# Kernel tuning notes

Measured on AMD Instinct MI355X. Metric: run time of the kernel, lower is better.

## Reference

```python
import jax, jax.numpy as jnp
import numpy as np

DECAY = 0.999
EPS = 1e-5
COMMIT = 0.25
ORTHO_W = 10.0
NUM_ORTHO = 128


def setup_inputs() -> dict:
    key = jax.random.key(0)
    k1, k2 = jax.random.split(key)
    M, D = 2048, 512
    B, T = 32, 1024
    x = jax.random.normal(k1, (B, T, D), dtype=jnp.float32)
    init_bound = 1.0 / M
    emb = jax.random.uniform(k2, (M, D), minval=-init_bound, maxval=init_bound, dtype=jnp.float32)
    return {
        "x": x,
        "embedding": emb,
        "ema_count": jnp.zeros((M,), jnp.float32),
        "ema_weight": emb,  # torch init: ema_weight = embedding.clone()
    }


def reference(x, embedding, ema_count, ema_weight):
    M, D = embedding.shape
    x_sg = jax.lax.stop_gradient(x)
    x_flat = x_sg.reshape(-1, D)  # [N, D]

    distances = (jnp.sum(embedding * embedding, axis=1)[None, :]
                 + jnp.sum(x_flat * x_flat, axis=1, keepdims=True)
                 - 2.0 * (x_flat @ embedding.T))
    indices = jnp.argmin(distances.astype(jnp.float32), axis=-1)  # [N]

    quantized = embedding[indices].reshape(x.shape)

    # EMA updates (training=True). one_hot(indices).sum(0) == scatter-add counts;
    # encodings.T @ x_flat == scatter-add of x rows into code slots.
    counts = jnp.zeros((M,), x.dtype).at[indices].add(1.0)
    new_count = DECAY * ema_count + (1.0 - DECAY) * counts
    n = jnp.sum(new_count)
    new_count = (new_count + EPS) / (n + M * EPS) * n
    dw = jnp.zeros((M, D), x.dtype).at[indices].add(x_flat)
    new_weight = DECAY * ema_weight + (1.0 - DECAY) * dw
    new_embedding = new_weight / new_count[:, None]

    codebook_loss = jnp.mean((x_sg - quantized) ** 2)
    e_latent_loss = jnp.mean((x - jax.lax.stop_gradient(quantized)) ** 2)
    commitment_loss = COMMIT * e_latent_loss

    quant_st = x + jax.lax.stop_gradient(quantized - x)  # straight-through

    # ortho loss over used codes of the UPDATED codebook (torch: self.embedding post-EMA).
    # Deterministic jit-safe variant of unique+randperm: take the first NUM_ORTHO
    # used code ids (stable argsort puts used codes first), mask padding if fewer.
    used = counts > 0
    order = jnp.argsort(jnp.where(used, 0, 1).astype(jnp.int32))  # stable sort
    sel = order[:NUM_ORTHO]
    valid = used[sel].astype(x.dtype)  # [NUM_ORTHO]
    codebk = new_embedding[sel]
    norm = jnp.maximum(jnp.linalg.norm(codebk, axis=-1, keepdims=True), 1e-12)
    normed = (codebk / norm) * valid[:, None]
    cosine_sim = normed @ normed.T
    n_valid = jnp.sum(valid)
    ortho_loss = jnp.sum((cosine_sim - jnp.diag(valid)) ** 2) / (n_valid * n_valid) * ORTHO_W

    return (quant_st, commitment_loss, codebook_loss, ortho_loss, indices,
            new_embedding, new_count, new_weight)
```

## Files before the change

kernel.cpp:

```cpp
#include <hip/hip_runtime.h>
#include <math.h>

#define N_ROWS 32768
#define M_CODES 2048
#define D_DIM 512
#define MARGIN 1.2e-3f
#define CAND_CAP 32

#define OUT_QST       0
#define OUT_COMMIT    16777216
#define OUT_CODEBOOK  16777217
#define OUT_ORTHO     16777218
#define OUT_INDICES   16777219
#define OUT_NEWEMB    16809987
#define OUT_NEWCOUNT  17858563
#define OUT_NEWW      17860611

#define WS_COUNTS     0
#define WS_CURSOR     2048
#define WS_SSE        4096
#define WS_ORTHO      4097
#define WS_CANDCNT    4104
#define WS_ZERO_FLOATS 36872
#define WS_E2         36872
#define WS_X2         38920
#define WS_IDX        71688
#define WS_NCN        104456
#define WS_SEL        106504
#define WS_VALID      106632
#define WS_NVALID     106760
#define WS_NORMED     106768
#define WS_NORMEDT    172304
#define WS_OFFS       237840
#define WS_ORDER      239896
#define WS_CANDC      272664
#define WS_CANDD      1321240
#define WS_XH         2369816
#define WS_EH         10758424
#define WS_TOTAL_FLOATS 11282712

typedef __attribute__((ext_vector_type(8))) short short8v;
typedef __attribute__((ext_vector_type(4))) float f32x4;

__device__ __forceinline__ unsigned short f2bf(float f) {
    unsigned u = __float_as_uint(f);
    unsigned r = (u + 0x7fffu + ((u >> 16) & 1u)) >> 16;
    return (unsigned short)r;
}

#define GLOAD16(g, s) __builtin_amdgcn_global_load_lds( \
    (const __attribute__((address_space(1))) void*)(g), \
    (__attribute__((address_space(3))) void*)(s), 16, 0, 0)

__global__ __launch_bounds__(256) void prep_kernel(const float* __restrict__ emb,
                                                   const float* __restrict__ x,
                                                   float* __restrict__ e2,
                                                   float* __restrict__ x2,
                                                   unsigned short* __restrict__ xh,
                                                   unsigned short* __restrict__ eh) {
    int row  = blockIdx.x * 4 + (threadIdx.x >> 6);
    int lane = threadIdx.x & 63;
    bool is_e = row < M_CODES;
    const float* src = is_e ? (emb + (size_t)row * D_DIM)
                            : (x + (size_t)(row - M_CODES) * D_DIM);
    unsigned short* dh = is_e ? (eh + (size_t)row * D_DIM)
                              : (xh + (size_t)(row - M_CODES) * D_DIM);
    float4 a = *(const float4*)(src + lane * 4);
    float4 b = *(const float4*)(src + 256 + lane * 4);
    float s = a.x*a.x + a.y*a.y + a.z*a.z + a.w*a.w
            + b.x*b.x + b.y*b.y + b.z*b.z + b.w*b.w;
#pragma unroll
    for (int o = 32; o > 0; o >>= 1) s += __shfl_xor(s, o, 64);

    ushort4 h0, h1;
    h0.x = f2bf(a.x); h0.y = f2bf(a.y); h0.z = f2bf(a.z); h0.w = f2bf(a.w);
    h1.x = f2bf(b.x); h1.y = f2bf(b.y); h1.z = f2bf(b.z); h1.w = f2bf(b.w);
    *(ushort4*)(dh + lane * 4)       = h0;
    *(ushort4*)(dh + 256 + lane * 4) = h1;

    if (lane == 0) {
        if (is_e) e2[row] = s;
        else      x2[row - M_CODES] = s;
    }
}

__global__ __launch_bounds__(256) void sq_kernel(const float* __restrict__ emb,
                                                 const float* __restrict__ x,
                                                 float* __restrict__ e2,
                                                 float* __restrict__ x2) {
    int row  = blockIdx.x * 4 + (threadIdx.x >> 6);
    int lane = threadIdx.x & 63;
    const float* src = (row < M_CODES) ? (emb + (size_t)row * D_DIM)
                                       : (x + (size_t)(row - M_CODES) * D_DIM);
    float4 a = *(const float4*)(src + lane * 4);
    float4 b = *(const float4*)(src + 256 + lane * 4);
    float s = a.x*a.x + a.y*a.y + a.z*a.z + a.w*a.w
            + b.x*b.x + b.y*b.y + b.z*b.z + b.w*b.w;
#pragma unroll
    for (int o = 32; o > 0; o >>= 1) s += __shfl_xor(s, o, 64);
    if (lane == 0) {
        if (row < M_CODES) e2[row] = s;
        else               x2[row - M_CODES] = s;
    }
}

__global__ __launch_bounds__(256, 1) void approx5_kernel(const unsigned short* __restrict__ xh,
                                                         const unsigned short* __restrict__ eh,
                                                         const float* __restrict__ e2g,
                                                         int* __restrict__ candcnt,
                                                         int* __restrict__ candC,
                                                         float* __restrict__ candD) {
    __shared__ short Bh[2][32768];

    const int t  = threadIdx.x;
    const int w  = t >> 6;
    const int l  = t & 63;
    const int ml = l & 15;
    const int q  = l >> 4;

    const int row0 = blockIdx.x * 128;
    const int wrow = row0 + w * 32;

    short8v af[2][16];
#pragma unroll
    for (int mi = 0; mi < 2; ++mi) {
        const unsigned short* ar = xh + (size_t)(wrow + mi * 16 + ml) * D_DIM + q * 8;
#pragma unroll
        for (int kk = 0; kk < 16; ++kk)
            af[mi][kk] = *(const short8v*)(ar + kk * 32);
    }

#define STAGE_B(buf, ch) do {                                                   \
    const int cb_ = (ch) * 64;                                                  \
    _Pragma("unroll")                                                           \
    for (int j_ = 0; j_ < 16; ++j_) {                                           \
        int c_ = w * 16 + j_;                                                   \
        GLOAD16(eh + (size_t)(cb_ + c_) * D_DIM + ((l ^ (c_ & 7)) * 8),         \
                &Bh[(buf)][c_ * 512]);                                          \
    }                                                                           \
} while (0)

    float rmin[2][4];
#pragma unroll
    for (int mi = 0; mi < 2; ++mi)
#pragma unroll
        for (int r = 0; r < 4; ++r) rmin[mi][r] = 3.0e38f;

    STAGE_B(0, 0);
    __syncthreads();
    int cur = 0;

    for (int ch = 0; ch < 32; ++ch) {
        if (ch < 31) STAGE_B(cur ^ 1, ch + 1);

        const int code0 = ch * 64;
        const short* Bb = &Bh[cur][0];

        f32x4 acc[2][4];
#pragma unroll
        for (int mi = 0; mi < 2; ++mi)
#pragma unroll
            for (int ni = 0; ni < 4; ++ni) acc[mi][ni] = (f32x4)0.f;

#pragma unroll
        for (int kk = 0; kk < 16; ++kk) {
#pragma unroll
            for (int ni = 0; ni < 4; ++ni) {
                const int c = ni * 16 + ml;
                short8v b = *(const short8v*)(Bb + c * 512 + (((kk * 4 + q) ^ (c & 7)) << 3));
                acc[0][ni] = __builtin_amdgcn_mfma_f32_16x16x32_bf16(af[0][kk], b, acc[0][ni], 0, 0, 0);
                acc[1][ni] = __builtin_amdgcn_mfma_f32_16x16x32_bf16(af[1][kk], b, acc[1][ni], 0, 0, 0);
            }
        }

        float e2v[4];
#pragma unroll
        for (int ni = 0; ni < 4; ++ni) e2v[ni] = e2g[code0 + ni * 16 + ml];

#pragma unroll
        for (int mi = 0; mi < 2; ++mi)
#pragma unroll
            for (int r = 0; r < 4; ++r) {
                float v = fminf(fminf(e2v[0] - 2.0f * acc[mi][0][r],
                                      e2v[1] - 2.0f * acc[mi][1][r]),
                                fminf(e2v[2] - 2.0f * acc[mi][2][r],
                                      e2v[3] - 2.0f * acc[mi][3][r]));
#pragma unroll
                for (int o = 1; o < 16; o <<= 1) v = fminf(v, __shfl_xor(v, o, 64));
                rmin[mi][r] = fminf(rmin[mi][r], v);
                const float rm = rmin[mi][r] + MARGIN;
                const int row_g = wrow + mi * 16 + q * 4 + r;
#pragma unroll
                for (int ni = 0; ni < 4; ++ni) {
                    float dd = e2v[ni] - 2.0f * acc[mi][ni][r];
                    if (dd <= rm) {
                        int pos = atomicAdd(&candcnt[row_g], 1);
                        if (pos < CAND_CAP) {
                            candC[row_g * CAND_CAP + pos] = code0 + ni * 16 + ml;
                            candD[row_g * CAND_CAP + pos] = dd;
                        }
                    }
                }
            }

        __syncthreads();
        cur ^= 1;
    }
#undef STAGE_B
}

__global__ __launch_bounds__(256) void rerank_kernel(const float* __restrict__ x,
                                                     const float* __restrict__ emb,
                                                     const float* __restrict__ e2,
                                                     const float* __restrict__ x2,
                                                     const int* __restrict__ candcnt,
                                                     const int* __restrict__ candC,
                                                     const float* __restrict__ candD,
                                                     float* __restrict__ counts,
                                                     int* __restrict__ idx_out,
                                                     float* __restrict__ idxf_out) {
    const int w = threadIdx.x >> 6;
    const int lane = threadIdx.x & 63;
    const int row = blockIdx.x * 4 + w;

    int cnt = candcnt[row];
    int best_c;

    if (cnt > CAND_CAP) {
        const float x2r = x2[row];
        const float* xr = x + (size_t)row * D_DIM;
        float bd = 3.0e38f;
        int   bc = 0x7fffffff;
        for (int c = lane; c < M_CODES; c += 64) {
            const float* er = emb + (size_t)c * D_DIM;
            float dot = 0.f;
            for (int k = 0; k < D_DIM; ++k) dot = fmaf(xr[k], er[k], dot);
            float d = (x2r + e2[c]) - 2.0f * dot;
            if (d < bd || (d == bd && c < bc)) { bd = d; bc = c; }
        }
#pragma unroll
        for (int o = 32; o > 0; o >>= 1) {
            float od = __shfl_xor(bd, o, 64);
            int   oc = __shfl_xor(bc, o, 64);
            if (od < bd || (od == bd && oc < bc)) { bd = od; bc = oc; }
        }
        best_c = bc;
    } else {
        float d = 3.0e38f;
        int   c = 0x7fffffff;
        if (lane < cnt) {
            d = candD[row * CAND_CAP + lane];
            c = candC[row * CAND_CAP + lane];
        }
        float dmin = d;
#pragma unroll
        for (int o = 32; o > 0; o >>= 1) dmin = fminf(dmin, __shfl_xor(dmin, o, 64));

        bool surv = (lane < cnt) && (d <= dmin + MARGIN);
        unsigned long long mask = __ballot(surv);

        if (__popcll(mask) == 1) {
            int src = __ffsll((long long)mask) - 1;
            best_c = __shfl(c, src, 64);
        } else {
            const float x2r = x2[row];
            const float* xr = x + (size_t)row * D_DIM;
            float4 xa = *(const float4*)(xr + lane * 8);
            float4 xb = *(const float4*)(xr + lane * 8 + 4);
            float bd = 3.0e38f;
            int   bc = 0x7fffffff;
            unsigned long long m = mask;
            while (m) {
                int src = __ffsll((long long)m) - 1;
                m &= m - 1;
                int cs = __shfl(c, src, 64);
                const float* er = emb + (size_t)cs * D_DIM;
                float4 ea = *(const float4*)(er + lane * 8);
                float4 eb = *(const float4*)(er + lane * 8 + 4);
                float dot = xa.x*ea.x + xa.y*ea.y + xa.z*ea.z + xa.w*ea.w
                          + xb.x*eb.x + xb.y*eb.y + xb.z*eb.z + xb.w*eb.w;
#pragma unroll
                for (int o = 32; o > 0; o >>= 1) dot += __shfl_xor(dot, o, 64);
                float t1 = x2r + e2[cs];
                float dex = t1 - 2.0f * dot;
                if (dex < bd || (dex == bd && cs < bc)) { bd = dex; bc = cs; }
            }
            best_c = bc;
        }
    }
    if (lane == 0) {
        idx_out[row] = best_c;
        idxf_out[row] = (float)best_c;
        atomicAdd(&counts[best_c], 1.0f);
    }
}

__global__ __launch_bounds__(256) void argmin_kernel(const float* __restrict__ x,
                                                     const float* __restrict__ emb,
                                                     const float* __restrict__ e2,
                                                     const float* __restrict__ x2,
                                                     int* __restrict__ idx_out,
                                                     float* __restrict__ idxf_out) {
    __shared__ float As[64][36];
    __shared__ float Bs[32][68];
    __shared__ float e2s[64];
    __shared__ float redD[64][17];
    __shared__ int   redI[64][17];

    const int t  = threadIdx.x;
    const int tx = t & 15;
    const int ty = t >> 4;
    const int row0 = blockIdx.x * 64;

    float rmin[4];
    int   ridx[4];
#pragma unroll
    for (int r = 0; r < 4; ++r) { rmin[r] = 3.0e38f; ridx[r] = 0; }

    float x2r[4];
#pragma unroll
    for (int r = 0; r < 4; ++r) x2r[r] = x2[row0 + ty * 4 + r];

    const int lr = t >> 3;
    const int lc = t & 7;

    for (int m0 = 0; m0 < M_CODES; m0 += 64) {
        __syncthreads();
        if (t < 64) e2s[t] = e2[m0 + t];

        float acc[4][4];
#pragma unroll
        for (int r = 0; r < 4; ++r)
#pragma unroll
            for (int c = 0; c < 4; ++c) acc[r][c] = 0.f;

        for (int k0 = 0; k0 < D_DIM; k0 += 32) {
            __syncthreads();
#pragma unroll
            for (int p = 0; p < 2; ++p) {
                int r = p * 32 + lr;
                float4 v = *(const float4*)(x + (size_t)(row0 + r) * D_DIM + k0 + lc * 4);
                *(float4*)(&As[r][lc * 4]) = v;
            }
#pragma unroll
            for (int p = 0; p < 2; ++p) {
                int r = p * 32 + lr;
                float4 v = *(const float4*)(emb + (size_t)(m0 + r) * D_DIM + k0 + lc * 4);
                Bs[lc * 4 + 0][r] = v.x;
                Bs[lc * 4 + 1][r] = v.y;
                Bs[lc * 4 + 2][r] = v.z;
                Bs[lc * 4 + 3][r] = v.w;
            }
            __syncthreads();

#pragma unroll
            for (int kk = 0; kk < 32; kk += 4) {
                float av[4][4], bv[4][4];
#pragma unroll
                for (int r = 0; r < 4; ++r) {
                    float4 a4 = *(const float4*)(&As[ty * 4 + r][kk]);
                    av[r][0] = a4.x; av[r][1] = a4.y; av[r][2] = a4.z; av[r][3] = a4.w;
                }
#pragma unroll
                for (int j = 0; j < 4; ++j) {
                    float4 b4 = *(const float4*)(&Bs[kk + j][tx * 4]);
                    bv[j][0] = b4.x; bv[j][1] = b4.y; bv[j][2] = b4.z; bv[j][3] = b4.w;
                }
#pragma unroll
                for (int j = 0; j < 4; ++j)
#pragma unroll
                    for (int r = 0; r < 4; ++r)
#pragma unroll
                        for (int c = 0; c < 4; ++c)
                            acc[r][c] += av[r][j] * bv[j][c];
            }
        }

#pragma unroll
        for (int c = 0; c < 4; ++c) {
            int mm = tx * 4 + c;
            int m  = m0 + mm;
            float e2v = e2s[mm];
#pragma unroll
            for (int r = 0; r < 4; ++r) {
                float t1 = x2r[r] + e2v;
                float dd  = t1 - 2.0f * acc[r][c];
                if (dd < rmin[r]) { rmin[r] = dd; ridx[r] = m; }
            }
        }
    }

    __syncthreads();
#pragma unroll
    for (int r = 0; r < 4; ++r) {
        redD[ty * 4 + r][tx] = rmin[r];
        redI[ty * 4 + r][tx] = ridx[r];
    }
    __syncthreads();
    if (t < 64) {
        float best = redD[t][0];
        int   bi   = redI[t][0];
#pragma unroll
        for (int i = 1; i < 16; ++i) {
            float dd = redD[t][i];
            int   ii = redI[t][i];
            if (dd < best || (dd == best && ii < bi)) { best = dd; bi = ii; }
        }
        idx_out[row0 + t]  = bi;
        idxf_out[row0 + t] = (float)bi;
    }
}

__global__ __launch_bounds__(256) void hist_kernel(const int* __restrict__ idx,
                                                   float* __restrict__ counts) {
    int r = blockIdx.x * 256 + threadIdx.x;
    atomicAdd(&counts[idx[r]], 1.0f);
}

__global__ __launch_bounds__(256) void qst_sse_kernel(const float* __restrict__ x,
                                                      const float* __restrict__ emb,
                                                      const int* __restrict__ idx,
                                                      float* __restrict__ sse,
                                                      float* __restrict__ qst) {
    const int w    = threadIdx.x >> 6;
    const int lane = threadIdx.x & 63;
    const int rowbase = blockIdx.x * 16 + w * 4;
    float loss = 0.f;
    for (int i = 0; i < 4; ++i) {
        const int row = rowbase + i;
        const int m   = idx[row];
#pragma unroll
        for (int j = 0; j < 2; ++j) {
            const int off = j * 256 + lane * 4;
            float4 xv = *(const float4*)(x + (size_t)row * D_DIM + off);
            float4 qv = *(const float4*)(emb + (size_t)m * D_DIM + off);
            float4 qs;
            qs.x = xv.x + (qv.x - xv.x);
            qs.y = xv.y + (qv.y - xv.y);
            qs.z = xv.z + (qv.z - xv.z);
            qs.w = xv.w + (qv.w - xv.w);
            *(float4*)(qst + (size_t)row * D_DIM + off) = qs;
            float dx;
            dx = xv.x - qv.x; loss += dx * dx;
            dx = xv.y - qv.y; loss += dx * dx;
            dx = xv.z - qv.z; loss += dx * dx;
            dx = xv.w - qv.w; loss += dx * dx;
        }
    }
#pragma unroll
    for (int o = 32; o > 0; o >>= 1) loss += __shfl_xor(loss, o, 64);
    if (lane == 0) atomicAdd(sse, loss);
}

__global__ __launch_bounds__(256) void f1_kernel(const float* __restrict__ ema_count,
                                                 const float* __restrict__ counts,
                                                 float* __restrict__ out_newcount,
                                                 float* __restrict__ nc_ws) {
    __shared__ float red[256];
    int t = threadIdx.x;
    float raw[8];
    float part = 0.f;
#pragma unroll
    for (int i = 0; i < 8; ++i) {
        int m = t * 8 + i;
        raw[i] = 0.999f * ema_count[m] + 0.001f * counts[m];
        part += raw[i];
    }
    red[t] = part;
    __syncthreads();
    for (int s = 128; s > 0; s >>= 1) {
        if (t < s) red[t] += red[t + s];
        __syncthreads();
    }
    float n = red[0];
    float denom = n + (float)M_CODES * 1e-5f;
#pragma unroll
    for (int i = 0; i < 8; ++i) {
        int m = t * 8 + i;
        float v = (raw[i] + 1e-5f) / denom * n;
        out_newcount[m] = v;
        nc_ws[m] = v;
    }
}

__global__ __launch_bounds__(256) void scan_kernel(const float* __restrict__ counts,
                                                   int* __restrict__ offs) {
    __shared__ int pre[257];
    int t = threadIdx.x;
    int c[8];
    int s = 0;
#pragma unroll
    for (int i = 0; i < 8; ++i) { c[i] = (int)counts[t * 8 + i]; s += c[i]; }
    pre[t] = s;
    __syncthreads();
    if (t == 0) {
        int run = 0;
        for (int i = 0; i < 256; ++i) { int v = pre[i]; pre[i] = run; run += v; }
        pre[256] = run;
    }
    __syncthreads();
    int base = pre[t];
#pragma unroll
    for (int i = 0; i < 8; ++i) { offs[t * 8 + i] = base; base += c[i]; }
}

__global__ __launch_bounds__(256) void fill_kernel(const int* __restrict__ idx,
                                                   const int* __restrict__ offs,
                                                   int* __restrict__ cursor,
                                                   int* __restrict__ order) {
    int r = blockIdx.x * 256 + threadIdx.x;
    int m = idx[r];
    int pos = atomicAdd(&cursor[m], 1);
    order[offs[m] + pos] = r;
}

__global__ __launch_bounds__(256) void gather_nw_kernel(const float* __restrict__ x,
                                                        const float* __restrict__ ema_weight,
                                                        const float* __restrict__ ncn,
                                                        const float* __restrict__ counts,
                                                        const int* __restrict__ offs,
                                                        const int* __restrict__ order,
                                                        float* __restrict__ out_ne,
                                                        float* __restrict__ out_nw) {
    const int m = blockIdx.x;
    const int t = threadIdx.x;
    const int beg = offs[m];
    const int end = beg + (int)counts[m];
    float ax = 0.f, ay = 0.f;
    for (int j = beg; j < end; ++j) {
        int r = order[j];
        float2 v = *(const float2*)(x + (size_t)r * D_DIM + t * 2);
        ax += v.x; ay += v.y;
    }
    size_t i = (size_t)m * D_DIM + t * 2;
    float2 wv = *(const float2*)(ema_weight + i);
    float  c  = ncn[m];
    float2 nw, ne;
    nw.x = 0.999f * wv.x + 0.001f * ax; ne.x = nw.x / c;
    nw.y = 0.999f * wv.y + 0.001f * ay; ne.y = nw.y / c;
    *(float2*)(out_nw + i) = nw;
    *(float2*)(out_ne + i) = ne;
}

__global__ __launch_bounds__(256) void g1_kernel(const float* __restrict__ counts,
                                                 const float* __restrict__ new_emb,
                                                 int* __restrict__ sel,
                                                 float* __restrict__ valid,
                                                 float* __restrict__ n_valid,
                                                 float* __restrict__ normed,
                                                 float* __restrict__ normedT) {
    __shared__ int pre[257];
    int t = threadIdx.x;
    int u = 0;
#pragma unroll
    for (int i = 0; i < 8; ++i) u += (counts[t * 8 + i] > 0.f) ? 1 : 0;
    pre[t] = u;
    __syncthreads();
    if (t == 0) {
        int run = 0;
        for (int i = 0; i < 256; ++i) { int c = pre[i]; pre[i] = run; run += c; }
        pre[256] = run;
    }
    __syncthreads();
    int U = pre[256];
    int base = pre[t];
    int run = 0;
    for (int i = 0; i < 8; ++i) {
        int m = t * 8 + i;
        bool used = counts[m] > 0.f;
        int ur = base + run;
        if (used) {
            if (ur < 128) sel[ur] = m;
            run++;
        } else {
            int pos = U + (m - ur);
            if (pos < 128) sel[pos] = m;
        }
    }
    __syncthreads();
    if (t < 128) valid[t] = (counts[sel[t]] > 0.f) ? 1.f : 0.f;
    __syncthreads();
    if (t == 0) {
        float s = 0.f;
        for (int i = 0; i < 128; ++i) s += valid[i];
        *n_valid = s;
    }
    int w = t >> 6, lane = t & 63;
    for (int r = w; r < 128; r += 4) {
        int sm = sel[r];
        const float* src = new_emb + (size_t)sm * D_DIM;
        float4 a = *(const float4*)(src + lane * 4);
        float4 b = *(const float4*)(src + 256 + lane * 4);
        float s = a.x*a.x + a.y*a.y + a.z*a.z + a.w*a.w
                + b.x*b.x + b.y*b.y + b.z*b.z + b.w*b.w;
#pragma unroll
        for (int o = 32; o > 0; o >>= 1) s += __shfl_xor(s, o, 64);
        float norm = fmaxf(sqrtf(s), 1e-12f);
        float vv = valid[r];
        float4 na, nb;
        na.x = a.x / norm * vv; na.y = a.y / norm * vv;
        na.z = a.z / norm * vv; na.w = a.w / norm * vv;
        nb.x = b.x / norm * vv; nb.y = b.y / norm * vv;
        nb.z = b.z / norm * vv; nb.w = b.w / norm * vv;
        *(float4*)(normed + (size_t)r * D_DIM + lane * 4) = na;
        *(float4*)(normed + (size_t)r * D_DIM + 256 + lane * 4) = nb;
        normedT[(lane * 4 + 0) * 128 + r] = na.x;
        normedT[(lane * 4 + 1) * 128 + r] = na.y;
        normedT[(lane * 4 + 2) * 128 + r] = na.z;
        normedT[(lane * 4 + 3) * 128 + r] = na.w;
        normedT[(256 + lane * 4 + 0) * 128 + r] = nb.x;
        normedT[(256 + lane * 4 + 1) * 128 + r] = nb.y;
        normedT[(256 + lane * 4 + 2) * 128 + r] = nb.z;
        normedT[(256 + lane * 4 + 3) * 128 + r] = nb.w;
    }
}

__global__ __launch_bounds__(128) void g2_kernel(const float* __restrict__ normed,
                                                 const float* __restrict__ normedT,
                                                 const float* __restrict__ valid,
                                                 float* __restrict__ ortho_acc) {
    __shared__ float rowi[512];
    __shared__ float red[128];
    int i = blockIdx.x, t = threadIdx.x;
    *(float4*)(rowi + t * 4) = *(const float4*)(normed + (size_t)i * D_DIM + t * 4);
    __syncthreads();
    float dot = 0.f;
    for (int k = 0; k < D_DIM; ++k) dot += rowi[k] * normedT[k * 128 + t];
    float diag = (i == t) ? valid[i] : 0.f;
    float d = dot - diag;
    red[t] = d * d;
    __syncthreads();
    for (int s = 64; s > 0; s >>= 1) {
        if (t < s) red[t] += red[t + s];
        __syncthreads();
    }
    if (t == 0) atomicAdd(ortho_acc, red[0]);
}

__global__ void g3_kernel(const float* __restrict__ sse,
                          const float* __restrict__ ortho_acc,
                          const float* __restrict__ n_valid,
                          float* __restrict__ out3) {
    if (threadIdx.x == 0 && blockIdx.x == 0) {
        float m = *sse / 16777216.f;
        out3[0] = 0.25f * m;
        out3[1] = m;
        float nv = *n_valid;
        out3[2] = *ortho_acc / (nv * nv) * 10.f;
    }
}

extern "C" void kernel_launch(void* const* d_in, const int* in_sizes, int n_in,
                              void* d_out, int out_size, void* d_ws, size_t ws_size,
                              hipStream_t stream) {
    const float* x          = (const float*)d_in[0];
    const float* emb        = (const float*)d_in[1];
    const float* ema_count  = (const float*)d_in[2];
    const float* ema_weight = (const float*)d_in[3];
    float* out = (float*)d_out;
    float* ws  = (float*)d_ws;

    float* counts  = ws + WS_COUNTS;
    int*   cursor  = (int*)(ws + WS_CURSOR);
    float* sse     = ws + WS_SSE;
    float* ortho   = ws + WS_ORTHO;
    int*   candcnt = (int*)(ws + WS_CANDCNT);
    float* e2      = ws + WS_E2;
    float* x2      = ws + WS_X2;
    int*   idxws   = (int*)(ws + WS_IDX);
    float* ncn     = ws + WS_NCN;
    int*   sel     = (int*)(ws + WS_SEL);
    float* valid   = ws + WS_VALID;
    float* nvalid  = ws + WS_NVALID;
    float* normed  = ws + WS_NORMED;
    float* normedT = ws + WS_NORMEDT;
    int*   offs    = (int*)(ws + WS_OFFS);
    int*   order   = (int*)(ws + WS_ORDER);
    int*   candC   = (int*)(ws + WS_CANDC);
    float* candD   = ws + WS_CANDD;
    unsigned short* xh = (unsigned short*)(ws + WS_XH);
    unsigned short* eh = (unsigned short*)(ws + WS_EH);

    const bool big_ws = ws_size >= (size_t)WS_TOTAL_FLOATS * sizeof(float);

    hipMemsetAsync(ws, 0, (size_t)WS_ZERO_FLOATS * sizeof(float), stream);

    if (big_ws) {
        prep_kernel<<<(M_CODES + N_ROWS) / 4, 256, 0, stream>>>(emb, x, e2, x2, xh, eh);
        approx5_kernel<<<N_ROWS / 128, 256, 0, stream>>>(xh, eh, e2, candcnt, candC, candD);
        rerank_kernel<<<N_ROWS / 4, 256, 0, stream>>>(x, emb, e2, x2, candcnt, candC, candD,
                                                      counts, idxws, out + OUT_INDICES);
    } else {
        sq_kernel<<<(M_CODES + N_ROWS) / 4, 256, 0, stream>>>(emb, x, e2, x2);
        argmin_kernel<<<N_ROWS / 64, 256, 0, stream>>>(x, emb, e2, x2, idxws,
                                                       out + OUT_INDICES);
        hist_kernel<<<N_ROWS / 256, 256, 0, stream>>>(idxws, counts);
    }

    qst_sse_kernel<<<N_ROWS / 16, 256, 0, stream>>>(x, emb, idxws, sse, out + OUT_QST);

    f1_kernel<<<1, 256, 0, stream>>>(ema_count, counts, out + OUT_NEWCOUNT, ncn);

    scan_kernel<<<1, 256, 0, stream>>>(counts, offs);

    fill_kernel<<<N_ROWS / 256, 256, 0, stream>>>(idxws, offs, cursor, order);

    gather_nw_kernel<<<M_CODES, 256, 0, stream>>>(x, ema_weight, ncn, counts, offs, order,
                                                  out + OUT_NEWEMB, out + OUT_NEWW);

    g1_kernel<<<1, 256, 0, stream>>>(counts, out + OUT_NEWEMB, sel, valid, nvalid,
                                     normed, normedT);

    g2_kernel<<<128, 128, 0, stream>>>(normed, normedT, valid, ortho);

    g3_kernel<<<1, 64, 0, stream>>>(sse, ortho, nvalid, out + OUT_COMMIT);
}
```

Before: 573.9 us.

## Split codebook across wave pairs in approximate distance kernel for higher occupancy

Result: slower. 592.5 us (+3.2%).

```diff
diff --git a/kernel.cpp b/kernel.cpp
--- a/kernel.cpp
+++ b/kernel.cpp
@@ -104,39 +104,44 @@
     }
 }
 
-__global__ __launch_bounds__(256, 1) void approx5_kernel(const unsigned short* __restrict__ xh,
+__global__ __launch_bounds__(256, 2) void approx6_kernel(const unsigned short* __restrict__ xh,
                                                          const unsigned short* __restrict__ eh,
                                                          const float* __restrict__ e2g,
                                                          int* __restrict__ candcnt,
                                                          int* __restrict__ candC,
                                                          float* __restrict__ candD) {
-    __shared__ short Bh[2][32768];
-
-    const int t  = threadIdx.x;
-    const int w  = t >> 6;
-    const int l  = t & 63;
-    const int ml = l & 15;
-    const int q  = l >> 4;
-
-    const int row0 = blockIdx.x * 128;
-    const int wrow = row0 + w * 32;
+    __shared__ short Bh[2][2][8192];
+
+    const int t    = threadIdx.x;
+    const int w    = t >> 6;
+    const int l    = t & 63;
+    const int ml   = l & 15;
+    const int q    = l >> 4;
+    const int half = w & 1;
+    const int rh   = w >> 1;
+
+    const int row0  = blockIdx.x * 64 + rh * 32;
+    const int cbase = half * 1024;
 
     short8v af[2][16];
 #pragma unroll
     for (int mi = 0; mi < 2; ++mi) {
-        const unsigned short* ar = xh + (size_t)(wrow + mi * 16 + ml) * D_DIM + q * 8;
+        const unsigned short* ar = xh + (size_t)(row0 + mi * 16 + ml) * D_DIM + q * 8;
 #pragma unroll
         for (int kk = 0; kk < 16; ++kk)
             af[mi][kk] = *(const short8v*)(ar + kk * 32);
     }
 
-#define STAGE_B(buf, ch) do {                                                   \
-    const int cb_ = (ch) * 64;                                                  \
+    const int c0   = rh * 8;
+    const int grow = l >> 3;
+    const int cs   = c0 + grow;
+    const int sp8  = ((l & 7) ^ (cs & 7)) * 8;
+
+#define STAGE(buf, ch) do {                                                     \
     _Pragma("unroll")                                                           \
-    for (int j_ = 0; j_ < 16; ++j_) {                                           \
-        int c_ = w * 16 + j_;                                                   \
-        GLOAD16(eh + (size_t)(cb_ + c_) * D_DIM + ((l ^ (c_ & 7)) * 8),         \
-                &Bh[(buf)][c_ * 512]);                                          \
+    for (int kb_ = 0; kb_ < 8; ++kb_) {                                         \
+        GLOAD16(eh + (size_t)(cbase + (ch) * 16 + cs) * D_DIM + kb_ * 64 + sp8, \
+                &Bh[half][(buf)][(kb_ * 16 + c0) * 64]);                        \
     }                                                                           \
 } while (0)
 
@@ -146,59 +151,46 @@
 #pragma unroll
         for (int r = 0; r < 4; ++r) rmin[mi][r] = 3.0e38f;
 
-    STAGE_B(0, 0);
+    STAGE(0, 0);
     __syncthreads();
     int cur = 0;
 
-    for (int ch = 0; ch < 32; ++ch) {
-        if (ch < 31) STAGE_B(cur ^ 1, ch + 1);
-
-        const int code0 = ch * 64;
-        const short* Bb = &Bh[cur][0];
-
-        f32x4 acc[2][4];
+    for (int ch = 0; ch < 64; ++ch) {
+        if (ch < 63) STAGE(cur ^ 1, ch + 1);
+
+        const int code0 = cbase + ch * 16;
+        const short* Bb = &Bh[half][cur][0];
+
+        f32x4 acc[2];
+        acc[0] = (f32x4)0.f;
+        acc[1] = (f32x4)0.f;
+
+#pragma unroll
+        for (int kk = 0; kk < 16; ++kk) {
+            short8v b = *(const short8v*)(Bb + ((kk >> 1) * 16 + ml) * 64
+                                             + (((4 * (kk & 1) + q) ^ (ml & 7)) << 3));
+            acc[0] = __builtin_amdgcn_mfma_f32_16x16x32_bf16(af[0][kk], b, acc[0], 0, 0, 0);
+            acc[1] = __builtin_amdgcn_mfma_f32_16x16x32_bf16(af[1][kk], b, acc[1], 0, 0, 0);
+        }
+
+        const float e2v = e2g[code0 + ml];
+
 #pragma unroll
         for (int mi = 0; mi < 2; ++mi)
 #pragma unroll
-            for (int ni = 0; ni < 4; ++ni) acc[mi][ni] = (f32x4)0.f;
-
-#pragma unroll
-        for (int kk = 0; kk < 16; ++kk) {
-#pragma unroll
-            for (int ni = 0; ni < 4; ++ni) {
-                const int c = ni * 16 + ml;
-                short8v b = *(const short8v*)(Bb + c * 512 + (((kk * 4 + q) ^ (c & 7)) << 3));
-                acc[0][ni] = __builtin_amdgcn_mfma_f32_16x16x32_bf16(af[0][kk], b, acc[0][ni], 0, 0, 0);
-                acc[1][ni] = __builtin_amdgcn_mfma_f32_16x16x32_bf16(af[1][kk], b, acc[1][ni], 0, 0, 0);
-            }
-        }
-
-        float e2v[4];
-#pragma unroll
-        for (int ni = 0; ni < 4; ++ni) e2v[ni] = e2g[code0 + ni * 16 + ml];
-
-#pragma unroll
-        for (int mi = 0; mi < 2; ++mi)
-#pragma unroll
             for (int r = 0; r < 4; ++r) {
-                float v = fminf(fminf(e2v[0] - 2.0f * acc[mi][0][r],
-                                      e2v[1] - 2.0f * acc[mi][1][r]),
-                                fminf(e2v[2] - 2.0f * acc[mi][2][r],
-                                      e2v[3] - 2.0f * acc[mi][3][r]));
+                float dd = e2v - 2.0f * acc[mi][r];
+                float v = dd;
 #pragma unroll
                 for (int o = 1; o < 16; o <<= 1) v = fminf(v, __shfl_xor(v, o, 64));
                 rmin[mi][r] = fminf(rmin[mi][r], v);
                 const float rm = rmin[mi][r] + MARGIN;
-                const int row_g = wrow + mi * 16 + q * 4 + r;
-#pragma unroll
-                for (int ni = 0; ni < 4; ++ni) {
-                    float dd = e2v[ni] - 2.0f * acc[mi][ni][r];
-                    if (dd <= rm) {
-                        int pos = atomicAdd(&candcnt[row_g], 1);
-                        if (pos < CAND_CAP) {
-                            candC[row_g * CAND_CAP + pos] = code0 + ni * 16 + ml;
-                            candD[row_g * CAND_CAP + pos] = dd;
-                        }
+                if (dd <= rm) {
+                    const int row_g = row0 + mi * 16 + q * 4 + r;
+                    int pos = atomicAdd(&candcnt[row_g], 1);
+                    if (pos < CAND_CAP) {
+                        candC[row_g * CAND_CAP + pos] = code0 + ml;
+                        candD[row_g * CAND_CAP + pos] = dd;
                     }
                 }
             }
@@ -206,7 +198,7 @@
         __syncthreads();
         cur ^= 1;
     }
-#undef STAGE_B
+#undef STAGE
 }
 
 __global__ __launch_bounds__(256) void rerank_kernel(const float* __restrict__ x,
@@ -687,7 +679,7 @@
 
     if (big_ws) {
         prep_kernel<<<(M_CODES + N_ROWS) / 4, 256, 0, stream>>>(emb, x, e2, x2, xh, eh);
-        approx5_kernel<<<N_ROWS / 128, 256, 0, stream>>>(xh, eh, e2, candcnt, candC, candD);
+        approx6_kernel<<<N_ROWS / 64, 256, 0, stream>>>(xh, eh, e2, candcnt, candC, candD);
         rerank_kernel<<<N_ROWS / 4, 256, 0, stream>>>(x, emb, e2, x2, candcnt, candC, candD,
                                                       counts, idxws, out + OUT_INDICES);
     } else {
```
